# Kernel optimization log

Measured on AMD Instinct MI355X. Metric: run time of the kernel, lower is better.

Reference implementation:

```python
import jax, jax.numpy as jnp
import numpy as np

FP8_MAX = 448.0  # max finite value of float8_e4m3fn


def quantize_tensorwise(x):
    """Tensorwise fp8 quantization: returns fp8 tensor and inverse scale."""
    amax = jnp.max(jnp.abs(x))
    inv_scale = jnp.maximum(amax, jnp.asarray(1e-12, x.dtype)) / FP8_MAX
    q = (x / inv_scale).astype(jnp.float8_e4m3fn)
    return q, inv_scale


def setup_inputs() -> dict:
    key = jax.random.key(0)
    k1, k2, k3 = jax.random.split(key, 3)
    x = jax.random.normal(k1, (4, 1024, 4096), dtype=jnp.float32)
    weight = jax.random.normal(k2, (4096, 4096), dtype=jnp.float32) * 0.02
    bias = jax.random.normal(k3, (4096,), dtype=jnp.float32)
    return {"x": x, "weight": weight, "bias": bias}


def reference(x, weight, bias):
    out_shape = (*x.shape[:-1], weight.shape[0])
    xm = x.reshape(-1, x.shape[-1])                    # [M, K]
    fp8_x, x_inv_scale = quantize_tensorwise(xm)       # fp8 input + tensorwise scale
    fp8_wt, w_inv_scale = quantize_tensorwise(weight.T)  # weight.t() quantized, [K, N]
    # fp8 GEMM with inline dequant: (fp8_x @ fp8_w.T) * sx * sw + bias
    acc = jnp.matmul(fp8_x.astype(jnp.float32), fp8_wt.astype(jnp.float32))
    out = acc * (x_inv_scale * w_inv_scale) + bias.astype(jnp.float32)
    return out.reshape(out_shape).astype(x.dtype)
```

## Files before the change

### kernel.cpp

```cpp
#include <hip/hip_runtime.h>
#include <hip/hip_bf16.h>
#include <stdint.h>

static constexpr int M = 4096, N = 4096, K = 4096;
static constexpr float FP8_MAX = 448.0f;

using f32x16 = __attribute__((ext_vector_type(16))) float;
using i32x4  = __attribute__((ext_vector_type(4))) int;
using i32x8  = __attribute__((ext_vector_type(8))) int;

static constexpr size_t AQ_OFF   = 0;
static constexpr size_t BQ_OFF   = (size_t)M * K;
static constexpr size_t AMAX_OFF = BQ_OFF + (size_t)N * K;

__global__ void init_amax_kernel(float* amax) {
    amax[0] = 0.0f;
    amax[1] = 0.0f;
}

__global__ __launch_bounds__(256) void amax_kernel(const float* __restrict__ x,
                                                   const float* __restrict__ w,
                                                   float* __restrict__ amax,
                                                   int n4_per_tensor,
                                                   int blocks_per_tensor) {
    const int tensor = blockIdx.x / blocks_per_tensor;
    const int blk    = blockIdx.x % blocks_per_tensor;
    const float4* src = (const float4*)(tensor == 0 ? x : w);

    float m = 0.0f;
    for (int i = blk * blockDim.x + threadIdx.x; i < n4_per_tensor;
         i += blocks_per_tensor * blockDim.x) {
        float4 v = src[i];
        m = fmaxf(m, fmaxf(fmaxf(fabsf(v.x), fabsf(v.y)),
                           fmaxf(fabsf(v.z), fabsf(v.w))));
    }
    #pragma unroll
    for (int off = 32; off >= 1; off >>= 1)
        m = fmaxf(m, __shfl_xor(m, off, 64));

    __shared__ float sm[4];
    const int lane = threadIdx.x & 63, wid = threadIdx.x >> 6;
    if (lane == 0) sm[wid] = m;
    __syncthreads();
    if (threadIdx.x == 0) {
        m = fmaxf(fmaxf(sm[0], sm[1]), fmaxf(sm[2], sm[3]));
        atomicMax((unsigned int*)&amax[tensor], __float_as_uint(m));
    }
}

__global__ __launch_bounds__(256) void quant_kernel(const float* __restrict__ x,
                                                    const float* __restrict__ w,
                                                    unsigned char* __restrict__ aq,
                                                    unsigned char* __restrict__ bq,
                                                    const float* __restrict__ amax,
                                                    int n4_per_tensor) {
    int gid = blockIdx.x * blockDim.x + threadIdx.x;
    const int tensor = (gid >= n4_per_tensor) ? 1 : 0;
    const int i = tensor ? gid - n4_per_tensor : gid;

    const float inv = fmaxf(amax[tensor], 1e-12f) / FP8_MAX;
    const float4* src = (const float4*)(tensor == 0 ? x : w);
    int* dst = (int*)(tensor == 0 ? aq : bq);

    float4 v = src[i];
    float q0 = v.x / inv, q1 = v.y / inv, q2 = v.z / inv, q3 = v.w / inv;
    int packed = __builtin_amdgcn_cvt_pk_fp8_f32(q0, q1, 0, false);
    packed     = __builtin_amdgcn_cvt_pk_fp8_f32(q2, q3, packed, true);
    dst[i] = packed;
}

static constexpr int BM = 256, BN = 256, BK = 64, DEPTH = 4, NT = K / BK;

__device__ __forceinline__ void gld_lds16(const void* g, void* l) {
    __builtin_amdgcn_global_load_lds(
        (const __attribute__((address_space(1))) void*)g,
        (__attribute__((address_space(3))) void*)l, 16, 0, 0);
}

struct Frags {
    i32x8 a[4];
    i32x8 b[2];
};

__global__ __launch_bounds__(512, 2) void gemm_kernel(const unsigned char* __restrict__ Aq,
                                                      const unsigned char* __restrict__ Bq,
                                                      const float* __restrict__ amax,
                                                      const float* __restrict__ bias,
                                                      float* __restrict__ out) {
    __shared__ unsigned char lds[DEPTH][2][BM * BK];

    const int tid  = threadIdx.x;
    const int lane = tid & 63;
    const int w    = tid >> 6;
    const int wr   = w >> 2, wc = w & 3;

    const int bid = blockIdx.x;
    const int swz = (bid & 7) * 32 + (bid >> 3);
    const int brow = (swz >> 4) * BM;
    const int bcol = (swz & 15) * BN;

    const float sx = fmaxf(amax[0], 1e-12f) / FP8_MAX;
    const float sw = fmaxf(amax[1], 1e-12f) / FP8_MAX;
    const float scale = sx * sw;

    const int r4    = lane >> 2;
    const int row0  = w * 16 + r4;
    const int chk   = ((lane & 3) ^ ((row0 >> 1) & 3)) * 16;
    const unsigned char* Abase = Aq + (size_t)brow * K;
    const unsigned char* Bbase = Bq + (size_t)bcol * K;

    const int frow = lane & 31;
    const int swzr = (frow >> 1) & 3;
    const int c0   = (lane >> 5) * 2;
    const int off0 = ((c0 ^ swzr) << 4);
    const int off1 = (((c0 + 1) ^ swzr) << 4);

    f32x16 acc[4][2] = {};

#define STAGE(t, d)                                                                            \
    do {                                                                                       \
        const size_t _k0 = (size_t)(t) * BK;                                                   \
        gld_lds16(Abase + (size_t)row0 * K + _k0 + chk,         &lds[d][0][w * 1024]);         \
        gld_lds16(Abase + (size_t)(row0 + 128) * K + _k0 + chk, &lds[d][0][8192 + w * 1024]);  \
        gld_lds16(Bbase + (size_t)row0 * K + _k0 + chk,         &lds[d][1][w * 1024]);         \
        gld_lds16(Bbase + (size_t)(row0 + 128) * K + _k0 + chk, &lds[d][1][8192 + w * 1024]);  \
    } while (0)

#define READ_FRAGS(F, rs)                                                      \
    do {                                                                       \
        const unsigned char* _Ab = &lds[rs][0][0];                             \
        const unsigned char* _Bb = &lds[rs][1][0];                             \
        _Pragma("unroll")                                                      \
        for (int _mt = 0; _mt < 4; ++_mt) {                                    \
            const unsigned char* _p = _Ab + (wr * 128 + _mt * 32 + frow) * BK; \
            i32x4 _lo = *(const i32x4*)(_p + off0);                            \
            i32x4 _hi = *(const i32x4*)(_p + off1);                            \
            F.a[_mt] = __builtin_shufflevector(_lo, _hi, 0, 1, 2, 3, 4, 5, 6, 7); \
        }                                                                      \
        _Pragma("unroll")                                                      \
        for (int _nt = 0; _nt < 2; ++_nt) {                                    \
            const unsigned char* _p = _Bb + (wc * 64 + _nt * 32 + frow) * BK;  \
            i32x4 _lo = *(const i32x4*)(_p + off0);                            \
            i32x4 _hi = *(const i32x4*)(_p + off1);                            \
            F.b[_nt] = __builtin_shufflevector(_lo, _hi, 0, 1, 2, 3, 4, 5, 6, 7); \
        }                                                                      \
    } while (0)

#define MFMA_ALL(F)                                                                 \
    do {                                                                            \
        __builtin_amdgcn_s_setprio(1);                                              \
        _Pragma("unroll")                                                           \
        for (int _mt = 0; _mt < 4; ++_mt)                                           \
            _Pragma("unroll")                                                       \
            for (int _nt = 0; _nt < 2; ++_nt)                                       \
                acc[_mt][_nt] = __builtin_amdgcn_mfma_scale_f32_32x32x64_f8f6f4(    \
                    F.a[_mt], F.b[_nt], acc[_mt][_nt], 0, 0, 0, 0x7F, 0, 0x7F);     \
        __builtin_amdgcn_s_setprio(0);                                              \
    } while (0)

#define ITER(t, CUR, NXT, rs, ss)                                              \
    do {                                                                       \
        STAGE(((t) + 3 < NT) ? (t) + 3 : NT - 1, ss);                          \
        READ_FRAGS(NXT, rs);                                                   \
        __builtin_amdgcn_sched_barrier(0);                                     \
        MFMA_ALL(CUR);                                                         \
        asm volatile("s_waitcnt lgkmcnt(0)" ::: "memory");                     \
        __builtin_amdgcn_sched_barrier(0);                                     \
        asm volatile("s_waitcnt vmcnt(4)" ::: "memory");                       \
        __builtin_amdgcn_s_barrier();                                          \
    } while (0)

    Frags fP, fQ;

    STAGE(0, 0);
    STAGE(1, 1);
    STAGE(2, 2);
    asm volatile("s_waitcnt vmcnt(8)" ::: "memory");
    __builtin_amdgcn_s_barrier();
    READ_FRAGS(fP, 0);
    asm volatile("s_waitcnt lgkmcnt(0)" ::: "memory");
    __builtin_amdgcn_sched_barrier(0);
    asm volatile("s_waitcnt vmcnt(4)" ::: "memory");
    __builtin_amdgcn_s_barrier();

    for (int t = 0; t < NT; t += 4) {
        ITER(t + 0, fP, fQ, 1, 3);
        ITER(t + 1, fQ, fP, 2, 0);
        ITER(t + 2, fP, fQ, 3, 1);
        ITER(t + 3, fQ, fP, 0, 2);
    }
#undef ITER
#undef MFMA_ALL
#undef READ_FRAGS
#undef STAGE

    #pragma unroll
    for (int mt = 0; mt < 4; ++mt) {
        const int rbase = brow + wr * 128 + mt * 32 + 4 * (lane >> 5);
        #pragma unroll
        for (int nt2 = 0; nt2 < 2; ++nt2) {
            const int col = bcol + wc * 64 + nt2 * 32 + (lane & 31);
            const float b = bias[col];
            #pragma unroll
            for (int reg = 0; reg < 16; ++reg) {
                const int row = rbase + (reg & 3) + 8 * (reg >> 2);
                out[(size_t)row * N + col] = acc[mt][nt2][reg] * scale + b;
            }
        }
    }
}

extern "C" void kernel_launch(void* const* d_in, const int* in_sizes, int n_in,
                              void* d_out, int out_size, void* d_ws, size_t ws_size,
                              hipStream_t stream) {
    const float* x    = (const float*)d_in[0];
    const float* w    = (const float*)d_in[1];
    const float* bias = (const float*)d_in[2];
    float* out = (float*)d_out;

    unsigned char* aq = (unsigned char*)d_ws + AQ_OFF;
    unsigned char* bq = (unsigned char*)d_ws + BQ_OFF;
    float* amax = (float*)((unsigned char*)d_ws + AMAX_OFF);

    const int n4 = (M * K) / 4;

    init_amax_kernel<<<1, 1, 0, stream>>>(amax);

    const int blocks_per_tensor = 512;
    amax_kernel<<<2 * blocks_per_tensor, 256, 0, stream>>>(x, w, amax, n4, blocks_per_tensor);

    const int quant_blocks = (2 * n4) / 256;
    quant_kernel<<<quant_blocks, 256, 0, stream>>>(x, w, aq, bq, amax, n4);

    gemm_kernel<<<256, 512, 0, stream>>>(aq, bq, amax, bias, out);
}
```

Before: 147.0 us.

## Load B fragments directly from global into registers, bypassing LDS

B tiles are no longer staged through LDS. Each wave loads its own B fragments from global memory straight into registers, two K-steps ahead through four rotating register sets, while A keeps the LDS pipeline. The LDS footprint and LDS read traffic for B shrink by half. The cost is higher VGPR pressure and duplicated global reads of B across the two wave rows, since B is no longer shared through LDS. The barrier and wait schedule is restructured, and the register-level double-buffering of A fragments is dropped.

```diff
diff --git a/kernel.cpp b/kernel.cpp
--- a/kernel.cpp
+++ b/kernel.cpp
@@ -77,17 +77,14 @@
         (__attribute__((address_space(3))) void*)l, 16, 0, 0);
 }
 
-struct Frags {
-    i32x8 a[4];
-    i32x8 b[2];
-};
+struct BReg { i32x4 lo0, hi0, lo1, hi1; };
 
 __global__ __launch_bounds__(512, 2) void gemm_kernel(const unsigned char* __restrict__ Aq,
                                                       const unsigned char* __restrict__ Bq,
                                                       const float* __restrict__ amax,
                                                       const float* __restrict__ bias,
                                                       float* __restrict__ out) {
-    __shared__ unsigned char lds[DEPTH][2][BM * BK];
+    __shared__ unsigned char lds[DEPTH][BM * BK];
 
     const int tid  = threadIdx.x;
     const int lane = tid & 63;
@@ -107,7 +104,6 @@
     const int row0  = w * 16 + r4;
     const int chk   = ((lane & 3) ^ ((row0 >> 1) & 3)) * 16;
     const unsigned char* Abase = Aq + (size_t)brow * K;
-    const unsigned char* Bbase = Bq + (size_t)bcol * K;
 
     const int frow = lane & 31;
     const int swzr = (frow >> 1) & 3;
@@ -115,84 +111,73 @@
     const int off0 = ((c0 ^ swzr) << 4);
     const int off1 = (((c0 + 1) ^ swzr) << 4);
 
+    const unsigned char* Bp0 = Bq + (size_t)(bcol + wc * 64 + frow) * K      + (lane >> 5) * 32;
+    const unsigned char* Bp1 = Bq + (size_t)(bcol + wc * 64 + 32 + frow) * K + (lane >> 5) * 32;
+
     f32x16 acc[4][2] = {};
 
-#define STAGE(t, d)                                                                            \
+#define STAGE_A(t, d)                                                                          \
     do {                                                                                       \
         const size_t _k0 = (size_t)(t) * BK;                                                   \
-        gld_lds16(Abase + (size_t)row0 * K + _k0 + chk,         &lds[d][0][w * 1024]);         \
-        gld_lds16(Abase + (size_t)(row0 + 128) * K + _k0 + chk, &lds[d][0][8192 + w * 1024]);  \
-        gld_lds16(Bbase + (size_t)row0 * K + _k0 + chk,         &lds[d][1][w * 1024]);         \
-        gld_lds16(Bbase + (size_t)(row0 + 128) * K + _k0 + chk, &lds[d][1][8192 + w * 1024]);  \
+        gld_lds16(Abase + (size_t)row0 * K + _k0 + chk,         &lds[d][w * 1024]);            \
+        gld_lds16(Abase + (size_t)(row0 + 128) * K + _k0 + chk, &lds[d][8192 + w * 1024]);     \
     } while (0)
 
-#define READ_FRAGS(F, rs)                                                      \
+#define GLOAD_B(t, BR)                                                         \
     do {                                                                       \
-        const unsigned char* _Ab = &lds[rs][0][0];                             \
-        const unsigned char* _Bb = &lds[rs][1][0];                             \
+        const size_t _kb = (size_t)(t) * BK;                                   \
+        BR.lo0 = *(const i32x4*)(Bp0 + _kb);                                   \
+        BR.hi0 = *(const i32x4*)(Bp0 + _kb + 16);                              \
+        BR.lo1 = *(const i32x4*)(Bp1 + _kb);                                   \
+        BR.hi1 = *(const i32x4*)(Bp1 + _kb + 16);                              \
+    } while (0)
+
+#define ITER(t, rs, ss, BRcur, BRld)                                           \
+    do {                                                                       \
+        asm volatile("s_waitcnt vmcnt(6)" ::: "memory");                       \
+        __builtin_amdgcn_s_barrier();                                          \
+        STAGE_A(((t) + 3 < NT) ? (t) + 3 : NT - 1, ss);                        \
+        GLOAD_B(((t) + 2 < NT) ? (t) + 2 : NT - 1, BRld);                      \
+        i32x8 _aF[4];                                                          \
         _Pragma("unroll")                                                      \
         for (int _mt = 0; _mt < 4; ++_mt) {                                    \
-            const unsigned char* _p = _Ab + (wr * 128 + _mt * 32 + frow) * BK; \
+            const unsigned char* _p = &lds[rs][(wr * 128 + _mt * 32 + frow) * BK]; \
             i32x4 _lo = *(const i32x4*)(_p + off0);                            \
             i32x4 _hi = *(const i32x4*)(_p + off1);                            \
-            F.a[_mt] = __builtin_shufflevector(_lo, _hi, 0, 1, 2, 3, 4, 5, 6, 7); \
+            _aF[_mt] = __builtin_shufflevector(_lo, _hi, 0, 1, 2, 3, 4, 5, 6, 7); \
         }                                                                      \
+        i32x8 _b0 = __builtin_shufflevector(BRcur.lo0, BRcur.hi0, 0, 1, 2, 3, 4, 5, 6, 7); \
+        i32x8 _b1 = __builtin_shufflevector(BRcur.lo1, BRcur.hi1, 0, 1, 2, 3, 4, 5, 6, 7); \
+        __builtin_amdgcn_s_setprio(1);                                         \
         _Pragma("unroll")                                                      \
-        for (int _nt = 0; _nt < 2; ++_nt) {                                    \
-            const unsigned char* _p = _Bb + (wc * 64 + _nt * 32 + frow) * BK;  \
-            i32x4 _lo = *(const i32x4*)(_p + off0);                            \
-            i32x4 _hi = *(const i32x4*)(_p + off1);                            \
-            F.b[_nt] = __builtin_shufflevector(_lo, _hi, 0, 1, 2, 3, 4, 5, 6, 7); \
+        for (int _mt = 0; _mt < 4; ++_mt) {                                    \
+            acc[_mt][0] = __builtin_amdgcn_mfma_scale_f32_32x32x64_f8f6f4(     \
+                _aF[_mt], _b0, acc[_mt][0], 0, 0, 0, 0x7F, 0, 0x7F);           \
+            acc[_mt][1] = __builtin_amdgcn_mfma_scale_f32_32x32x64_f8f6f4(     \
+                _aF[_mt], _b1, acc[_mt][1], 0, 0, 0, 0x7F, 0, 0x7F);           \
         }                                                                      \
-    } while (0)
-
-#define MFMA_ALL(F)                                                                 \
-    do {                                                                            \
-        __builtin_amdgcn_s_setprio(1);                                              \
-        _Pragma("unroll")                                                           \
-        for (int _mt = 0; _mt < 4; ++_mt)                                           \
-            _Pragma("unroll")                                                       \
-            for (int _nt = 0; _nt < 2; ++_nt)                                       \
-                acc[_mt][_nt] = __builtin_amdgcn_mfma_scale_f32_32x32x64_f8f6f4(    \
-                    F.a[_mt], F.b[_nt], acc[_mt][_nt], 0, 0, 0, 0x7F, 0, 0x7F);     \
-        __builtin_amdgcn_s_setprio(0);                                              \
-    } while (0)
-
-#define ITER(t, CUR, NXT, rs, ss)                                              \
-    do {                                                                       \
-        STAGE(((t) + 3 < NT) ? (t) + 3 : NT - 1, ss);                          \
-        READ_FRAGS(NXT, rs);                                                   \
-        __builtin_amdgcn_sched_barrier(0);                                     \
-        MFMA_ALL(CUR);                                                         \
+        __builtin_amdgcn_s_setprio(0);                                         \
         asm volatile("s_waitcnt lgkmcnt(0)" ::: "memory");                     \
         __builtin_amdgcn_sched_barrier(0);                                     \
-        asm volatile("s_waitcnt vmcnt(4)" ::: "memory");                       \
-        __builtin_amdgcn_s_barrier();                                          \
     } while (0)
 
-    Frags fP, fQ;
-
-    STAGE(0, 0);
-    STAGE(1, 1);
-    STAGE(2, 2);
-    asm volatile("s_waitcnt vmcnt(8)" ::: "memory");
-    __builtin_amdgcn_s_barrier();
-    READ_FRAGS(fP, 0);
-    asm volatile("s_waitcnt lgkmcnt(0)" ::: "memory");
-    __builtin_amdgcn_sched_barrier(0);
-    asm volatile("s_waitcnt vmcnt(4)" ::: "memory");
-    __builtin_amdgcn_s_barrier();
+    BReg br0, br1, br2, br3;
+
+    STAGE_A(0, 0);
+    GLOAD_B(0, br0);
+    STAGE_A(1, 1);
+    GLOAD_B(1, br1);
+    STAGE_A(2, 2);
 
     for (int t = 0; t < NT; t += 4) {
-        ITER(t + 0, fP, fQ, 1, 3);
-        ITER(t + 1, fQ, fP, 2, 0);
-        ITER(t + 2, fP, fQ, 3, 1);
-        ITER(t + 3, fQ, fP, 0, 2);
+        ITER(t + 0, 0, 3, br0, br2);
+        ITER(t + 1, 1, 0, br1, br3);
+        ITER(t + 2, 2, 1, br2, br0);
+        ITER(t + 3, 3, 2, br3, br1);
     }
 #undef ITER
-#undef MFMA_ALL
-#undef READ_FRAGS
-#undef STAGE
+#undef GLOAD_B
+#undef STAGE_A
 
     #pragma unroll
     for (int mt = 0; mt < 4; ++mt) {
```

Result: slower. 162.5 us (+10.5%).

## Split each k-step into two half-phases with interleaved LDS reads and MFMAs

Applied to the files above, without the earlier changes.

Replaces the double-buffered register fragment ping-pong, which read the next tile's fragments while running MFMAs on the current one, with a per-iteration schedule. Each iteration reads B and half of A, issues the global prefetch, runs four MFMAs, then reads the other half of A and runs four more. The goal is to cut register pressure from holding two full fragment sets, and to add extra workgroup barriers so the two waves per SIMD stay in lockstep phases. In exchange, LDS read latency is no longer hidden behind a previous iteration's MFMAs, there are more barriers per k-step, and the vmcnt wait now allows 8 loads outstanding instead of 4.

```diff
diff --git a/kernel.cpp b/kernel.cpp
--- a/kernel.cpp
+++ b/kernel.cpp
@@ -77,11 +77,6 @@
         (__attribute__((address_space(3))) void*)l, 16, 0, 0);
 }
 
-struct Frags {
-    i32x8 a[4];
-    i32x8 b[2];
-};
-
 __global__ __launch_bounds__(512, 2) void gemm_kernel(const unsigned char* __restrict__ Aq,
                                                       const unsigned char* __restrict__ Bq,
                                                       const float* __restrict__ amax,
@@ -126,72 +121,65 @@
         gld_lds16(Bbase + (size_t)(row0 + 128) * K + _k0 + chk, &lds[d][1][8192 + w * 1024]);  \
     } while (0)
 
-#define READ_FRAGS(F, rs)                                                      \
+#define READ_FRAG(F, base_row, rs, ab)                                         \
     do {                                                                       \
-        const unsigned char* _Ab = &lds[rs][0][0];                             \
-        const unsigned char* _Bb = &lds[rs][1][0];                             \
-        _Pragma("unroll")                                                      \
-        for (int _mt = 0; _mt < 4; ++_mt) {                                    \
-            const unsigned char* _p = _Ab + (wr * 128 + _mt * 32 + frow) * BK; \
-            i32x4 _lo = *(const i32x4*)(_p + off0);                            \
-            i32x4 _hi = *(const i32x4*)(_p + off1);                            \
-            F.a[_mt] = __builtin_shufflevector(_lo, _hi, 0, 1, 2, 3, 4, 5, 6, 7); \
-        }                                                                      \
-        _Pragma("unroll")                                                      \
-        for (int _nt = 0; _nt < 2; ++_nt) {                                    \
-            const unsigned char* _p = _Bb + (wc * 64 + _nt * 32 + frow) * BK;  \
-            i32x4 _lo = *(const i32x4*)(_p + off0);                            \
-            i32x4 _hi = *(const i32x4*)(_p + off1);                            \
-            F.b[_nt] = __builtin_shufflevector(_lo, _hi, 0, 1, 2, 3, 4, 5, 6, 7); \
-        }                                                                      \
+        const unsigned char* _p = &lds[rs][ab][((base_row) + frow) * BK];      \
+        i32x4 _lo = *(const i32x4*)(_p + off0);                                \
+        i32x4 _hi = *(const i32x4*)(_p + off1);                                \
+        F = __builtin_shufflevector(_lo, _hi, 0, 1, 2, 3, 4, 5, 6, 7);         \
     } while (0)
 
-#define MFMA_ALL(F)                                                                 \
-    do {                                                                            \
-        __builtin_amdgcn_s_setprio(1);                                              \
-        _Pragma("unroll")                                                           \
-        for (int _mt = 0; _mt < 4; ++_mt)                                           \
-            _Pragma("unroll")                                                       \
-            for (int _nt = 0; _nt < 2; ++_nt)                                       \
-                acc[_mt][_nt] = __builtin_amdgcn_mfma_scale_f32_32x32x64_f8f6f4(    \
-                    F.a[_mt], F.b[_nt], acc[_mt][_nt], 0, 0, 0, 0x7F, 0, 0x7F);     \
-        __builtin_amdgcn_s_setprio(0);                                              \
+#define MXMFMA(a, b, c) \
+    __builtin_amdgcn_mfma_scale_f32_32x32x64_f8f6f4((a), (b), (c), 0, 0, 0, 0x7F, 0, 0x7F)
+
+#define ITER(t, rs, ss)                                                        \
+    do {                                                                       \
+        i32x8 _b0, _b1, _a0, _a1, _a2, _a3;                                    \
+                                                 \
+        READ_FRAG(_b0, wc * 64 +  0, rs, 1);                                   \
+        READ_FRAG(_b1, wc * 64 + 32, rs, 1);                                   \
+        READ_FRAG(_a0, wr * 128 +  0, rs, 0);                                  \
+        READ_FRAG(_a1, wr * 128 + 32, rs, 0);                                  \
+        STAGE(((t) + 3 < NT) ? (t) + 3 : NT - 1, ss);                          \
+        __builtin_amdgcn_s_barrier();                                          \
+        asm volatile("s_waitcnt lgkmcnt(0)" ::: "memory");                     \
+        __builtin_amdgcn_s_setprio(1);                                         \
+        acc[0][0] = MXMFMA(_a0, _b0, acc[0][0]);                               \
+        acc[0][1] = MXMFMA(_a0, _b1, acc[0][1]);                               \
+        acc[1][0] = MXMFMA(_a1, _b0, acc[1][0]);                               \
+        acc[1][1] = MXMFMA(_a1, _b1, acc[1][1]);                               \
+        __builtin_amdgcn_s_setprio(0);                                         \
+        __builtin_amdgcn_s_barrier();                                          \
+                                                 \
+        READ_FRAG(_a2, wr * 128 + 64, rs, 0);                                  \
+        READ_FRAG(_a3, wr * 128 + 96, rs, 0);                                  \
+        __builtin_amdgcn_s_barrier();                                          \
+        asm volatile("s_waitcnt lgkmcnt(0)" ::: "memory");                     \
+        __builtin_amdgcn_s_setprio(1);                                         \
+        acc[2][0] = MXMFMA(_a2, _b0, acc[2][0]);                               \
+        acc[2][1] = MXMFMA(_a2, _b1, acc[2][1]);                               \
+        acc[3][0] = MXMFMA(_a3, _b0, acc[3][0]);                               \
+        acc[3][1] = MXMFMA(_a3, _b1, acc[3][1]);                               \
+        __builtin_amdgcn_s_setprio(0);                                         \
+        asm volatile("s_waitcnt vmcnt(8)" ::: "memory");                       \
+        __builtin_amdgcn_s_barrier();                                          \
     } while (0)
-
-#define ITER(t, CUR, NXT, rs, ss)                                              \
-    do {                                                                       \
-        STAGE(((t) + 3 < NT) ? (t) + 3 : NT - 1, ss);                          \
-        READ_FRAGS(NXT, rs);                                                   \
-        __builtin_amdgcn_sched_barrier(0);                                     \
-        MFMA_ALL(CUR);                                                         \
-        asm volatile("s_waitcnt lgkmcnt(0)" ::: "memory");                     \
-        __builtin_amdgcn_sched_barrier(0);                                     \
-        asm volatile("s_waitcnt vmcnt(4)" ::: "memory");                       \
-        __builtin_amdgcn_s_barrier();                                          \
-    } while (0)
-
-    Frags fP, fQ;
 
     STAGE(0, 0);
     STAGE(1, 1);
     STAGE(2, 2);
     asm volatile("s_waitcnt vmcnt(8)" ::: "memory");
     __builtin_amdgcn_s_barrier();
-    READ_FRAGS(fP, 0);
-    asm volatile("s_waitcnt lgkmcnt(0)" ::: "memory");
-    __builtin_amdgcn_sched_barrier(0);
-    asm volatile("s_waitcnt vmcnt(4)" ::: "memory");
-    __builtin_amdgcn_s_barrier();
 
     for (int t = 0; t < NT; t += 4) {
-        ITER(t + 0, fP, fQ, 1, 3);
-        ITER(t + 1, fQ, fP, 2, 0);
-        ITER(t + 2, fP, fQ, 3, 1);
-        ITER(t + 3, fQ, fP, 0, 2);
+        ITER(t + 0, 0, 3);
+        ITER(t + 1, 1, 0);
+        ITER(t + 2, 2, 1);
+        ITER(t + 3, 3, 2);
     }
 #undef ITER
-#undef MFMA_ALL
-#undef READ_FRAGS
+#undef MXMFMA
+#undef READ_FRAG
 #undef STAGE
 
     #pragma unroll
```

Result: faster. 134.5 us (-8.5%).
